# Kernel tuning notes

Measured on AMD Instinct MI355X. Metric: run time of the kernel, lower is better.

## Reference

```python
import jax, jax.numpy as jnp
import numpy as np

B, S, HID = 2, 2048, 2048
H, KVH, D = 16, 4, 128
GROUPS = H // KVH
THETA = 10000.0
SCALE = 1.0 / np.sqrt(D).astype(np.float32)
NEG = -1e9


def setup_inputs() -> dict:
    key = jax.random.key(0)
    ks = jax.random.split(key, 6)
    x = jax.random.normal(ks[0], (B, S, HID), dtype=jnp.float32)
    # causal additive mask, broadcast over heads
    causal = jnp.triu(jnp.full((S, S), NEG, dtype=jnp.float32), k=1)
    attn_mask = jnp.broadcast_to(causal, (B, 1, S, S))
    pos_ids = jnp.broadcast_to(jnp.arange(S, dtype=jnp.int32), (B, S))
    sd = 0.02
    Wq = jax.random.normal(ks[1], (H * D, HID), dtype=jnp.float32) * sd
    Wk = jax.random.normal(ks[2], (KVH * D, HID), dtype=jnp.float32) * sd
    Wv = jax.random.normal(ks[3], (KVH * D, HID), dtype=jnp.float32) * sd
    Wo = jax.random.normal(ks[4], (HID, H * D), dtype=jnp.float32) * sd
    return {"x": x, "attn_mask": attn_mask, "pos_ids": pos_ids,
            "Wq": Wq, "Wk": Wk, "Wv": Wv, "Wo": Wo}


def _rope_cos_sin(pos_ids):
    # pos_ids: [B, S] -> cos/sin: [B, 1, S, D]
    inv_freq = 1.0 / (THETA ** (jnp.arange(0, D, 2, dtype=jnp.float32) / D))
    freqs = pos_ids.astype(jnp.float32)[:, :, None] * inv_freq  # [B, S, D/2]
    emb = jnp.concatenate([freqs, freqs], axis=-1)              # [B, S, D]
    return jnp.cos(emb)[:, None], jnp.sin(emb)[:, None]


def _rotate_half(t):
    t1, t2 = jnp.split(t, 2, axis=-1)
    return jnp.concatenate([-t2, t1], axis=-1)


def reference(x, attn_mask, pos_ids, Wq, Wk, Wv, Wo):
    b, s, _ = x.shape
    q = jnp.einsum('bsh,oh->bso', x, Wq).reshape(b, s, H, D).transpose(0, 2, 1, 3)
    k = jnp.einsum('bsh,oh->bso', x, Wk).reshape(b, s, KVH, D).transpose(0, 2, 1, 3)
    v = jnp.einsum('bsh,oh->bso', x, Wv).reshape(b, s, KVH, D).transpose(0, 2, 1, 3)
    cos, sin = _rope_cos_sin(pos_ids)
    q = q * cos + _rotate_half(q) * sin
    k = k * cos + _rotate_half(k) * sin
    # GQA: repeat kv heads
    k = jnp.repeat(k, GROUPS, axis=1)  # [b, H, s, D]
    v = jnp.repeat(v, GROUPS, axis=1)
    scores = jnp.einsum('bhqd,bhkd->bhqk', q, k) * SCALE + attn_mask
    weights = jax.nn.softmax(scores, axis=-1)  # dropout p=0 (eval)
    out = jnp.einsum('bhqk,bhkd->bhqd', weights, v)
    out = out.transpose(0, 2, 1, 3).reshape(b, s, H * D)
    return jnp.einsum('bso,ho->bsh', out, Wo)
```

## Files before the change

kernel.cpp:

```cpp
#include <hip/hip_runtime.h>
#include <hip/hip_bf16.h>
#include <stdint.h>

#define B_   2
#define S_   2048
#define HID_ 2048
#define H_   16
#define KVH_ 4
#define D_   128
#define SCALE_ 0.08838834764831845f
#define QSC_ (SCALE_ * 1.4426950408889634f)

typedef __attribute__((ext_vector_type(8))) short bf16x8;
typedef __attribute__((ext_vector_type(4))) float f32x4;
typedef __attribute__((ext_vector_type(4))) short short4v;

__device__ __forceinline__ void async_copy16(void* lds, const void* g) {
  __builtin_amdgcn_global_load_lds((__attribute__((address_space(1))) void*)(uintptr_t)g,
                                   (__attribute__((address_space(3))) void*)lds, 16, 0, 0);
}

__device__ __forceinline__ short bf16bits(float f) {
  __hip_bfloat16 t = __float2bfloat16(f);
  return __builtin_bit_cast(short, t);
}
__device__ __forceinline__ float bf16tof(short s) {
  return __bfloat162float(__builtin_bit_cast(__hip_bfloat16, s));
}

__global__ __launch_bounds__(256) void f2b_all(const float4* __restrict__ x,
                                               const float4* __restrict__ wq,
                                               const float4* __restrict__ wk,
                                               const float4* __restrict__ wv,
                                               const float4* __restrict__ wo,
                                               short4v* __restrict__ xb,
                                               short4v* __restrict__ wqb,
                                               short4v* __restrict__ wkb,
                                               short4v* __restrict__ wvb,
                                               short4v* __restrict__ wob) {
  int i = blockIdx.x * blockDim.x + threadIdx.x;
  const float4* src; short4v* dst; int off;
  if (i < 2097152)      { src = x;  dst = xb;  off = 0; }
  else if (i < 3145728) { src = wq; dst = wqb; off = 2097152; }
  else if (i < 3407872) { src = wk; dst = wkb; off = 3145728; }
  else if (i < 3670016) { src = wv; dst = wvb; off = 3407872; }
  else                  { src = wo; dst = wob; off = 3670016; }
  int k = i - off;
  float4 v = src[k];
  short4v o;
  o[0] = bf16bits(v.x); o[1] = bf16bits(v.y);
  o[2] = bf16bits(v.z); o[3] = bf16bits(v.w);
  dst[k] = o;
}

template <int MODE>
__global__ __launch_bounds__(256) void gemm_bt(const __hip_bfloat16* __restrict__ A,
                                               const __hip_bfloat16* __restrict__ Bw,
                                               void* __restrict__ Cout,
                                               void* __restrict__ Cout2,
                                               void* __restrict__ Cout3,
                                               int M, int N, int K) {
  __shared__ __align__(16) __hip_bfloat16 Asm[128 * 32];
  __shared__ __align__(16) __hip_bfloat16 Bsm[128 * 32];
  const int tid  = threadIdx.x;
  const int lane = tid & 63;
  const int wid  = tid >> 6;
  const int nwg = gridDim.x * gridDim.y;
  const int id  = blockIdx.y * gridDim.x + blockIdx.x;
  const int swz = (id & 7) * (nwg >> 3) + (id >> 3);
  const int m0 = (swz / gridDim.x) * 128;
  const int n0 = (swz % gridDim.x) * 128;
  const int qm = (wid >> 1) * 64;
  const int qn = (wid & 1) * 64;
  const int ar = lane & 15;
  const int ak = (lane >> 4) * 8;
  const int sr = tid >> 2;
  const int sc = (tid & 3) * 8;

  f32x4 acc[4][4] = {};

  for (int k0 = 0; k0 < K; k0 += 32) {
    async_copy16(&Asm[tid * 8],        A + (size_t)(m0 + sr) * K + k0 + sc);
    async_copy16(&Asm[2048 + tid * 8], A + (size_t)(m0 + 64 + sr) * K + k0 + sc);
    async_copy16(&Bsm[tid * 8],        Bw + (size_t)(n0 + sr) * K + k0 + sc);
    async_copy16(&Bsm[2048 + tid * 8], Bw + (size_t)(n0 + 64 + sr) * K + k0 + sc);
    __syncthreads();

    bf16x8 af[4], bfr[4];
#pragma unroll
    for (int i = 0; i < 4; ++i)
      af[i] = *(const bf16x8*)(&Asm[(qm + i * 16 + ar) * 32 + ak]);
#pragma unroll
    for (int j = 0; j < 4; ++j)
      bfr[j] = *(const bf16x8*)(&Bsm[(qn + j * 16 + ar) * 32 + ak]);
#pragma unroll
    for (int i = 0; i < 4; ++i)
#pragma unroll
      for (int j = 0; j < 4; ++j)
        acc[i][j] = __builtin_amdgcn_mfma_f32_16x16x32_bf16(af[i], bfr[j], acc[i][j], 0, 0, 0);
    __syncthreads();
  }

  const int rb = (lane >> 4) * 4;
  const int cl = lane & 15;
#pragma unroll
  for (int i = 0; i < 4; ++i)
#pragma unroll
    for (int j = 0; j < 4; ++j) {
      const int n = n0 + qn + j * 16 + cl;
#pragma unroll
      for (int r = 0; r < 4; ++r) {
        const int m = m0 + qm + i * 16 + rb + r;
        float v = acc[i][j][r];
        if (MODE == 3) {
          ((float*)Cout)[(size_t)m * N + n] = v;
        } else {
          const int bb = m >> 11, ss = m & (S_ - 1);
          if (n < 2048) {
            const int hh = n >> 7, dd = n & 127;
            ((__hip_bfloat16*)Cout)[(((size_t)bb * 16 + hh) * S_ + ss) * D_ + dd] = __float2bfloat16(v);
          } else if (n < 2560) {
            const int n2 = n - 2048, hh = n2 >> 7, dd = n2 & 127;
            ((__hip_bfloat16*)Cout2)[(((size_t)bb * 4 + hh) * S_ + ss) * D_ + dd] = __float2bfloat16(v);
          } else {
            const int n2 = n - 2560, hh = n2 >> 7, dd = n2 & 127;
            ((__hip_bfloat16*)Cout3)[(((size_t)bb * 4 + hh) * D_ + dd) * S_ + ss] = __float2bfloat16(v);
          }
        }
      }
    }
}

__global__ __launch_bounds__(256) void rope_inplace(__hip_bfloat16* __restrict__ buf,
                                                    const int* __restrict__ pos_ids,
                                                    int lognh, float scale) {
  int idx = blockIdx.x * blockDim.x + threadIdx.x;
  int t  = idx & 15;
  int s  = (idx >> 4) & (S_ - 1);
  int bh = idx >> 15;
  int b  = bh >> lognh;
  float pos = (float)pos_ids[b * S_ + s];
  size_t base = ((size_t)bh * S_ + s) * D_ + t * 4;
  short4v lo = *(short4v*)(buf + base);
  short4v hi = *(short4v*)(buf + base + 64);
  short4v lo2, hi2;
#pragma unroll
  for (int e = 0; e < 4; ++e) {
    float d = (float)(t * 4 + e);
    float ang = pos * exp2f(d * -0.20762050593046014f);
    float c = cosf(ang), sn = sinf(ang);
    float lv = bf16tof(lo[e]), hv = bf16tof(hi[e]);
    lo2[e] = bf16bits((lv * c - hv * sn) * scale);
    hi2[e] = bf16bits((hv * c + lv * sn) * scale);
  }
  *(short4v*)(buf + base)      = lo2;
  *(short4v*)(buf + base + 64) = hi2;
}

__global__ __launch_bounds__(512, 4) void flash_attn5(const __hip_bfloat16* __restrict__ Q,
                                                      const __hip_bfloat16* __restrict__ K,
                                                      const __hip_bfloat16* __restrict__ Vt,
                                                      const int* __restrict__ pos_ids,
                                                      __hip_bfloat16* __restrict__ O) {
  __shared__ __align__(16) __hip_bfloat16 Ksm[2][64 * 128];
  __shared__ __align__(16) __hip_bfloat16 Vsm[2][128 * 64];
  __shared__ __align__(16) __hip_bfloat16 Psm[8][16 * 64];
  const int tid  = threadIdx.x;
  const int lane = tid & 63;
  const int wid  = tid >> 6;
  const int i   = blockIdx.x;
  const int xcd = i & 7;
  const int j   = i >> 3;
  const int bh  = xcd * 4 + (j & 3);
  const int qt  = 15 - (j >> 2);
  const int b   = bh >> 4;
  const int h   = bh & 15;
  const int kvh = h >> 2;
  const int qrow0 = qt * 128 + wid * 16;
  const int ar = lane & 15;
  const int ag = lane >> 4;
  const int q  = qrow0 + ar;
  const int nkv = 2 * qt + 2;

  const __hip_bfloat16* Qb = Q  + ((size_t)bh * S_ + qrow0) * D_;
  const __hip_bfloat16* Kb = K  + (size_t)(b * KVH_ + kvh) * S_ * D_;
  const __hip_bfloat16* Vb = Vt + (size_t)(b * KVH_ + kvh) * D_ * S_;

  bf16x8 qf[4];
#pragma unroll
  for (int kf = 0; kf < 4; ++kf)
    qf[kf] = *(const bf16x8*)(Qb + (size_t)ar * D_ + kf * 32 + ag * 8);

  {
    const float posf = (float)pos_ids[b * S_ + q];
#pragma unroll
    for (int kf = 0; kf < 2; ++kf) {
      bf16x8 lo = qf[kf], hi = qf[kf + 2];
      bf16x8 nlo, nhi;
#pragma unroll
      for (int e = 0; e < 8; ++e) {
        const float d = (float)(kf * 32 + ag * 8 + e);
        const float ang = posf * exp2f(d * -0.20762050593046014f);
        const float c = cosf(ang), sn = sinf(ang);
        const float lv = bf16tof(lo[e]), hv = bf16tof(hi[e]);
        nlo[e] = bf16bits((lv * c - hv * sn) * QSC_);
        nhi[e] = bf16bits((hv * c + lv * sn) * QSC_);
      }
      qf[kf] = nlo; qf[kf + 2] = nhi;
    }
  }

  auto STAGE = [&](int sb, int t) {
    const int kv0 = t * 64;
#pragma unroll
    for (int c = 0; c < 2; ++c) {
      const int rK = c * 32 + (tid >> 4);
      const int cK = (tid & 15) ^ (rK & 7);
      async_copy16(&Ksm[sb][(c * 512 + tid) * 8],
                   Kb + (size_t)(kv0 + rK) * D_ + cK * 8);
      const int rV = c * 64 + (tid >> 3);
      const int cV = (tid & 7) ^ (rV & 7);
      async_copy16(&Vsm[sb][(c * 512 + tid) * 8],
                   Vb + (size_t)rV * S_ + kv0 + cV * 8);
    }
  };

  f32x4 acc[8] = {};
  float m = -1e30f, l = 0.f;
  char* pb = (char*)&Psm[wid][0];

  STAGE(0, 0);
  asm volatile("s_waitcnt vmcnt(0)" ::: "memory");
  __syncthreads();

  int buf = 0;
  for (int t = 0; t < nkv; ++t, buf ^= 1) {
    if (t + 1 < nkv) STAGE(buf ^ 1, t + 1);
    if (qrow0 + 15 >= 64 * t) {
      const int kv0 = t * 64;
      f32x4 st[4] = {};
      const char* kbase = (const char*)&Ksm[buf][0];
      __builtin_amdgcn_s_setprio(1);
#pragma unroll
      for (int kvt = 0; kvt < 4; ++kvt) {
        const int rr = kvt * 16 + ar;
        const int rx = rr & 7;
#pragma unroll
        for (int kf = 0; kf < 4; ++kf) {
          const bf16x8 kfrag = *(const bf16x8*)(kbase + rr * 256 + (((kf * 4 + ag) ^ rx) << 4));
          st[kvt] = __builtin_amdgcn_mfma_f32_16x16x32_bf16(kfrag, qf[kf], st[kvt], 0, 0, 0);
        }
      }
      __builtin_amdgcn_s_setprio(0);
      const bool needmask = (64 * t + 63 > qrow0);
      float sv[4][4];
      float mb = -3.0e38f;
#pragma unroll
      for (int kvt = 0; kvt < 4; ++kvt)
#pragma unroll
        for (int r = 0; r < 4; ++r) {
          float s = st[kvt][r];
          if (needmask) {
            const int kvi = kv0 + kvt * 16 + ag * 4 + r;
            if (kvi > q) s = -3.0e38f;
          }
          sv[kvt][r] = s;
          mb = fmaxf(mb, s);
        }
      mb = fmaxf(mb, __shfl_xor(mb, 16, 64));
      mb = fmaxf(mb, __shfl_xor(mb, 32, 64));
      if (!__all(mb - m <= 8.f)) {
        const float mnew = fmaxf(m, mb);
        const float sf = exp2f(m - mnew);
        m = mnew;
        l *= sf;
#pragma unroll
        for (int df = 0; df < 8; ++df)
#pragma unroll
          for (int r = 0; r < 4; ++r)
            acc[df][r] *= sf;
      }
      float psum = 0.f;
#pragma unroll
      for (int kvt = 0; kvt < 4; ++kvt) {
        short4v pk;
#pragma unroll
        for (int r = 0; r < 4; ++r) {
          const float p = exp2f(sv[kvt][r] - m);
          psum += p;
          pk[r] = bf16bits(p);
        }
        const int g = kvt * 2 + (ag >> 1);
        *(short4v*)(pb + ar * 128 + ((g ^ (ar & 7)) << 4) + (ag & 1) * 8) = pk;
      }
      psum += __shfl_xor(psum, 16, 64);
      psum += __shfl_xor(psum, 32, 64);
      l += psum;
      asm volatile("s_waitcnt lgkmcnt(0)" ::: "memory");
      const bf16x8 pf0 = *(const bf16x8*)(pb + ar * 128 + ((ag ^ (ar & 7)) << 4));
      const bf16x8 pf1 = *(const bf16x8*)(pb + ar * 128 + (((4 + ag) ^ (ar & 7)) << 4));
      const char* vbase = (const char*)&Vsm[buf][0];
      __builtin_amdgcn_s_setprio(1);
#pragma unroll
      for (int df = 0; df < 8; ++df) {
        const int rr = df * 16 + ar;
        const int rx = rr & 7;
        const bf16x8 v0 = *(const bf16x8*)(vbase + rr * 128 + ((ag ^ rx) << 4));
        const bf16x8 v1 = *(const bf16x8*)(vbase + rr * 128 + (((4 + ag) ^ rx) << 4));
        acc[df] = __builtin_amdgcn_mfma_f32_16x16x32_bf16(v0, pf0, acc[df], 0, 0, 0);
        acc[df] = __builtin_amdgcn_mfma_f32_16x16x32_bf16(v1, pf1, acc[df], 0, 0, 0);
      }
      __builtin_amdgcn_s_setprio(0);
    }
    asm volatile("s_waitcnt vmcnt(0)" ::: "memory");
    __syncthreads();
  }

  const float linv = 1.f / l;
  __hip_bfloat16* Ob = O + ((size_t)b * S_ + qrow0 + ar) * (H_ * D_) + h * D_;
#pragma unroll
  for (int df = 0; df < 8; ++df) {
    short4v o4;
#pragma unroll
    for (int r = 0; r < 4; ++r)
      o4[r] = bf16bits(acc[df][r] * linv);
    *(short4v*)(Ob + df * 16 + ag * 4) = o4;
  }
}

extern "C" void kernel_launch(void* const* d_in, const int* in_sizes, int n_in,
                              void* d_out, int out_size, void* d_ws, size_t ws_size,
                              hipStream_t stream) {
  (void)in_sizes; (void)n_in; (void)out_size; (void)ws_size;
  const float* x  = (const float*)d_in[0];
  const int* pos  = (const int*)d_in[2];
  const float* Wq = (const float*)d_in[3];
  const float* Wk = (const float*)d_in[4];
  const float* Wv = (const float*)d_in[5];
  const float* Wo = (const float*)d_in[6];

  char* ws = (char*)d_ws;
  __hip_bfloat16* xb   = (__hip_bfloat16*)(ws);
  __hip_bfloat16* wqb  = (__hip_bfloat16*)(ws + 16777216);
  __hip_bfloat16* wkb  = (__hip_bfloat16*)(ws + 25165824);
  __hip_bfloat16* wvb  = (__hip_bfloat16*)(ws + 27262976);
  __hip_bfloat16* wob  = (__hip_bfloat16*)(ws + 29360128);
  __hip_bfloat16* qb16 = (__hip_bfloat16*)(ws + 37748736);
  __hip_bfloat16* kb16 = (__hip_bfloat16*)(ws + 54525952);
  __hip_bfloat16* vt16 = (__hip_bfloat16*)(ws + 58720256);
  __hip_bfloat16* attn = (__hip_bfloat16*)(ws + 62914560);

  f2b_all<<<18432, 256, 0, stream>>>((const float4*)x, (const float4*)Wq, (const float4*)Wk,
                                     (const float4*)Wv, (const float4*)Wo,
                                     (short4v*)xb, (short4v*)wqb, (short4v*)wkb,
                                     (short4v*)wvb, (short4v*)wob);

  gemm_bt<5><<<dim3(24, 32), 256, 0, stream>>>(xb, wqb, qb16, kb16, vt16, 4096, 3072, 2048);

  rope_inplace<<<1024, 256, 0, stream>>>(kb16, pos, 2, 1.0f);

  flash_attn5<<<512, 512, 0, stream>>>(qb16, kb16, vt16, pos, attn);

  gemm_bt<3><<<dim3(16, 32), 256, 0, stream>>>(attn, wob, d_out, nullptr, nullptr, 4096, 2048, 2048);
}
```

Baseline: 243.3 us.

## Pair causal query tiles per block to balance flash-attention work

The flash attention kernel now uses 256-thread blocks that each process two 64-row query tiles, a short one (pair) and a long one (31-pair), one after the other. This gives every block the same amount of causal work. It also removes the wasted iterations where some warps skipped fully masked KV tiles inside 128-row tiles. The first KV tile for the second phase is prefetched during the last iteration of the first phase. The cost is that fewer warps share each staged K/V tile, which raises LDS traffic per unit of work, and the block does its two phases serially.

```diff
diff --git a/kernel.cpp b/kernel.cpp
--- a/kernel.cpp
+++ b/kernel.cpp
@@ -157,86 +157,89 @@
   *(short4v*)(buf + base + 64) = hi2;
 }
 
-__global__ __launch_bounds__(512, 4) void flash_attn5(const __hip_bfloat16* __restrict__ Q,
+__global__ __launch_bounds__(256, 2) void flash_attn6(const __hip_bfloat16* __restrict__ Q,
                                                       const __hip_bfloat16* __restrict__ K,
                                                       const __hip_bfloat16* __restrict__ Vt,
                                                       const int* __restrict__ pos_ids,
                                                       __hip_bfloat16* __restrict__ O) {
   __shared__ __align__(16) __hip_bfloat16 Ksm[2][64 * 128];
   __shared__ __align__(16) __hip_bfloat16 Vsm[2][128 * 64];
-  __shared__ __align__(16) __hip_bfloat16 Psm[8][16 * 64];
+  __shared__ __align__(16) __hip_bfloat16 Psm[4][16 * 64];
   const int tid  = threadIdx.x;
   const int lane = tid & 63;
   const int wid  = tid >> 6;
-  const int i   = blockIdx.x;
-  const int xcd = i & 7;
-  const int j   = i >> 3;
-  const int bh  = xcd * 4 + (j & 3);
-  const int qt  = 15 - (j >> 2);
-  const int b   = bh >> 4;
-  const int h   = bh & 15;
-  const int kvh = h >> 2;
-  const int qrow0 = qt * 128 + wid * 16;
+  const int i    = blockIdx.x;
+  const int xcd  = i & 7;
+  const int j    = i >> 3;
+  const int bh   = xcd * 4 + (j & 3);
+  const int pair = j >> 2;
+  const int b    = bh >> 4;
+  const int h    = bh & 15;
+  const int kvh  = h >> 2;
   const int ar = lane & 15;
   const int ag = lane >> 4;
-  const int q  = qrow0 + ar;
-  const int nkv = 2 * qt + 2;
-
-  const __hip_bfloat16* Qb = Q  + ((size_t)bh * S_ + qrow0) * D_;
+
   const __hip_bfloat16* Kb = K  + (size_t)(b * KVH_ + kvh) * S_ * D_;
   const __hip_bfloat16* Vb = Vt + (size_t)(b * KVH_ + kvh) * D_ * S_;
 
-  bf16x8 qf[4];
-#pragma unroll
-  for (int kf = 0; kf < 4; ++kf)
-    qf[kf] = *(const bf16x8*)(Qb + (size_t)ar * D_ + kf * 32 + ag * 8);
-
-  {
-    const float posf = (float)pos_ids[b * S_ + q];
-#pragma unroll
-    for (int kf = 0; kf < 2; ++kf) {
-      bf16x8 lo = qf[kf], hi = qf[kf + 2];
-      bf16x8 nlo, nhi;
-#pragma unroll
-      for (int e = 0; e < 8; ++e) {
-        const float d = (float)(kf * 32 + ag * 8 + e);
-        const float ang = posf * exp2f(d * -0.20762050593046014f);
-        const float c = cosf(ang), sn = sinf(ang);
-        const float lv = bf16tof(lo[e]), hv = bf16tof(hi[e]);
-        nlo[e] = bf16bits((lv * c - hv * sn) * QSC_);
-        nhi[e] = bf16bits((hv * c + lv * sn) * QSC_);
-      }
-      qf[kf] = nlo; qf[kf + 2] = nhi;
-    }
-  }
-
-  auto STAGE = [&](int sb, int t) {
-    const int kv0 = t * 64;
-#pragma unroll
-    for (int c = 0; c < 2; ++c) {
-      const int rK = c * 32 + (tid >> 4);
-      const int cK = (tid & 15) ^ (rK & 7);
-      async_copy16(&Ksm[sb][(c * 512 + tid) * 8],
-                   Kb + (size_t)(kv0 + rK) * D_ + cK * 8);
-      const int rV = c * 64 + (tid >> 3);
-      const int cV = (tid & 7) ^ (rV & 7);
-      async_copy16(&Vsm[sb][(c * 512 + tid) * 8],
-                   Vb + (size_t)rV * S_ + kv0 + cV * 8);
+  auto STAGE = [&](int sb, int kv0) {
+#pragma unroll
+    for (int c = 0; c < 4; ++c) {
+      const int idx = wid * 4 + c;
+      const int rowK = idx * 4 + (lane >> 4);
+      const int gcK  = (lane & 15) ^ (rowK & 7);
+      async_copy16(&Ksm[sb][idx * 512 + lane * 8],
+                   Kb + (size_t)(kv0 + rowK) * D_ + gcK * 8);
+      const int rowV = idx * 8 + (lane >> 3);
+      const int gcV  = (lane & 7) ^ (rowV & 7);
+      async_copy16(&Vsm[sb][idx * 512 + lane * 8],
+                   Vb + (size_t)rowV * S_ + kv0 + gcV * 8);
     }
   };
 
-  f32x4 acc[8] = {};
-  float m = -1e30f, l = 0.f;
   char* pb = (char*)&Psm[wid][0];
+  int buf = 0;
 
   STAGE(0, 0);
   asm volatile("s_waitcnt vmcnt(0)" ::: "memory");
   __syncthreads();
 
-  int buf = 0;
-  for (int t = 0; t < nkv; ++t, buf ^= 1) {
-    if (t + 1 < nkv) STAGE(buf ^ 1, t + 1);
-    if (qrow0 + 15 >= 64 * t) {
+#pragma unroll
+  for (int phase = 0; phase < 2; ++phase) {
+    const int qt    = phase ? (31 - pair) : pair;
+    const int qrow0 = qt * 64 + wid * 16;
+    const int q     = qrow0 + ar;
+
+    bf16x8 qf[4];
+    {
+      const __hip_bfloat16* Qb = Q + ((size_t)bh * S_ + qrow0) * D_;
+#pragma unroll
+      for (int kf = 0; kf < 4; ++kf)
+        qf[kf] = *(const bf16x8*)(Qb + (size_t)ar * D_ + kf * 32 + ag * 8);
+      const float posf = (float)pos_ids[b * S_ + q];
+#pragma unroll
+      for (int kf = 0; kf < 2; ++kf) {
+        bf16x8 lo = qf[kf], hi = qf[kf + 2];
+        bf16x8 nlo, nhi;
+#pragma unroll
+        for (int e = 0; e < 8; ++e) {
+          const float d = (float)(kf * 32 + ag * 8 + e);
+          const float ang = posf * exp2f(d * -0.20762050593046014f);
+          const float c = cosf(ang), sn = sinf(ang);
+          const float lv = bf16tof(lo[e]), hv = bf16tof(hi[e]);
+          nlo[e] = bf16bits((lv * c - hv * sn) * QSC_);
+          nhi[e] = bf16bits((hv * c + lv * sn) * QSC_);
+        }
+        qf[kf] = nlo; qf[kf + 2] = nhi;
+      }
+    }
+
+    f32x4 acc[8] = {};
+    float m = -1e30f, l = 0.f;
+
+    for (int t = 0; t <= qt; ++t) {
+      if (t < qt)            STAGE(buf ^ 1, (t + 1) * 64);
+      else if (phase == 0)   STAGE(buf ^ 1, 0);
       const int kv0 = t * 64;
       f32x4 st[4] = {};
       const char* kbase = (const char*)&Ksm[buf][0];
@@ -252,19 +255,15 @@
         }
       }
       __builtin_amdgcn_s_setprio(0);
-      const bool needmask = (64 * t + 63 > qrow0);
-      float sv[4][4];
+      const bool needmask = (t == qt);
       float mb = -3.0e38f;
 #pragma unroll
       for (int kvt = 0; kvt < 4; ++kvt)
 #pragma unroll
         for (int r = 0; r < 4; ++r) {
           float s = st[kvt][r];
-          if (needmask) {
-            const int kvi = kv0 + kvt * 16 + ag * 4 + r;
-            if (kvi > q) s = -3.0e38f;
-          }
-          sv[kvt][r] = s;
+          if (needmask && (kv0 + kvt * 16 + ag * 4 + r > q)) s = -3.0e38f;
+          st[kvt][r] = s;
           mb = fmaxf(mb, s);
         }
       mb = fmaxf(mb, __shfl_xor(mb, 16, 64));
@@ -286,7 +285,7 @@
         short4v pk;
 #pragma unroll
         for (int r = 0; r < 4; ++r) {
-          const float p = exp2f(sv[kvt][r] - m);
+          const float p = exp2f(st[kvt][r] - m);
           psum += p;
           pk[r] = bf16bits(p);
         }
@@ -311,20 +310,21 @@
         acc[df] = __builtin_amdgcn_mfma_f32_16x16x32_bf16(v1, pf1, acc[df], 0, 0, 0);
       }
       __builtin_amdgcn_s_setprio(0);
-    }
-    asm volatile("s_waitcnt vmcnt(0)" ::: "memory");
-    __syncthreads();
-  }
-
-  const float linv = 1.f / l;
-  __hip_bfloat16* Ob = O + ((size_t)b * S_ + qrow0 + ar) * (H_ * D_) + h * D_;
-#pragma unroll
-  for (int df = 0; df < 8; ++df) {
-    short4v o4;
-#pragma unroll
-    for (int r = 0; r < 4; ++r)
-      o4[r] = bf16bits(acc[df][r] * linv);
-    *(short4v*)(Ob + df * 16 + ag * 4) = o4;
+      asm volatile("s_waitcnt vmcnt(0)" ::: "memory");
+      __syncthreads();
+      buf ^= 1;
+    }
+
+    const float linv = 1.f / l;
+    __hip_bfloat16* Ob = O + ((size_t)b * S_ + qrow0 + ar) * (H_ * D_) + h * D_;
+#pragma unroll
+    for (int df = 0; df < 8; ++df) {
+      short4v o4;
+#pragma unroll
+      for (int r = 0; r < 4; ++r)
+        o4[r] = bf16bits(acc[df][r] * linv);
+      *(short4v*)(Ob + df * 16 + ag * 4) = o4;
+    }
   }
 }
 
@@ -359,7 +359,7 @@
 
   rope_inplace<<<1024, 256, 0, stream>>>(kb16, pos, 2, 1.0f);
 
-  flash_attn5<<<512, 512, 0, stream>>>(qb16, kb16, vt16, pos, attn);
+  flash_attn6<<<512, 256, 0, stream>>>(qb16, kb16, vt16, pos, attn);
 
   gemm_bt<3><<<dim3(16, 32), 256, 0, stream>>>(attn, wob, d_out, nullptr, nullptr, 4096, 2048, 2048);
 }
```

After: 228.4 us. -6.1%, faster.
